# Kernel optimization log

Hardware: AMD Instinct MI355X
Metric: run time of the kernel (lower is better)

Reference implementation:

```python
import jax, jax.numpy as jnp
import numpy as np

EPS = 1e-5
SLOPE = 0.01  # LeakyReLU default negative_slope
D_STATE = 16


def leaky(x):
    return jnp.where(x >= 0, x, SLOPE * x)


def instance_norm(x):
    # InstanceNorm3d(affine=False): normalize per (n, c) over spatial dims
    m = x.mean(axis=(2, 3, 4), keepdims=True)
    v = x.var(axis=(2, 3, 4), keepdims=True)
    return (x - m) * jax.lax.rsqrt(v + EPS)


def conv3d(x, w, b, groups=1, pad=0):
    y = jax.lax.conv_general_dilated(
        x, w, (1, 1, 1), [(pad, pad)] * 3,
        dimension_numbers=('NCDHW', 'OIDHW', 'NCDHW'),
        feature_group_count=groups)
    return y + b[None, :, None, None, None]


def conv_transpose2(x, w, b):
    # ConvTranspose3d(k=2, s=2): non-overlapping, so it is a pure einsum+interleave
    # x: [n,c,d,h,w], w: [c,o,2,2,2] (torch layout)
    y = jnp.einsum('ncdhw,coijk->nodihjwk', x, w)
    n, o, d, _, h, _, ww, _ = y.shape
    return y.reshape(n, o, 2 * d, 2 * h, 2 * ww) + b[None, :, None, None, None]


def selective_scan(u, dt, A, B, C, D):
    # u, dt: [b,l,d]; A: [d,n]; B, C: [b,l,n]; D: [d]
    dA = jnp.exp(dt[..., None] * A)                              # [b,l,d,n]
    dBu = dt[..., None] * B[:, :, None, :] * u[..., None]        # [b,l,d,n]

    def step(h, inp):
        dA_t, dBu_t, C_t = inp
        h = dA_t * h + dBu_t                                     # [b,d,n]
        y = jnp.einsum('bdn,bn->bd', h, C_t)
        return h, y

    h0 = jnp.zeros((u.shape[0],) + A.shape, u.dtype)
    _, ys = jax.lax.scan(
        step, h0,
        (dA.transpose(1, 0, 2, 3), dBu.transpose(1, 0, 2, 3), C.transpose(1, 0, 2)))
    return ys.transpose(1, 0, 2) + u * D                         # [b,l,d]


def mamba_block(x, in_proj_w, conv1d_w, conv1d_b, x_proj_w,
                dt_proj_w, dt_proj_b, A_log, D_param, out_proj_w):
    # x: [b,l,c]
    dt_rank = dt_proj_w.shape[1]
    xz = x @ in_proj_w.T                                         # [b,l,2*d_inner]
    xi, z = jnp.split(xz, 2, axis=-1)
    # causal depthwise conv1d over sequence (torch pads d_conv-1 both sides, keeps [:L])
    xi_c = xi.transpose(0, 2, 1)                                 # [b,d_inner,l]
    xi_c = jax.lax.conv_general_dilated(
        xi_c, conv1d_w, (1,), [(conv1d_w.shape[-1] - 1, 0)],
        dimension_numbers=('NCH', 'OIH', 'NCH'),
        feature_group_count=xi_c.shape[1])
    xi = jax.nn.silu(xi_c + conv1d_b[None, :, None]).transpose(0, 2, 1)  # [b,l,d_inner]
    x_dbl = xi @ x_proj_w.T
    dt, B, C = jnp.split(x_dbl, [dt_rank, dt_rank + D_STATE], axis=-1)
    dt = jax.nn.softplus(dt @ dt_proj_w.T + dt_proj_b)
    A = -jnp.exp(A_log)
    y = selective_scan(xi, dt, A, B, C, D_param)
    y = y * jax.nn.silu(z)
    return y @ out_proj_w.T


def layer_norm(x, w, b):
    m = x.mean(-1, keepdims=True)
    v = x.var(-1, keepdims=True)
    return (x - m) * jax.lax.rsqrt(v + EPS) * w + b


def up_forward(x1, x2, up_w, up_b, dc1_w, dc1_b, dc2_w, dc2_b, dc3_w, dc3_b,
               ln_w, ln_b, in_proj_w, conv1d_w, conv1d_b, x_proj_w,
               dt_proj_w, dt_proj_b, A_log, D_param, out_proj_w):
    x1 = conv_transpose2(x1, up_w, up_b)
    dZ = x2.shape[2] - x1.shape[2]
    dY = x2.shape[3] - x1.shape[3]
    dX = x2.shape[4] - x1.shape[4]
    x1 = jnp.pad(x1, ((0, 0), (0, 0),
                      (dZ // 2, dZ - dZ // 2),
                      (dY // 2, dY - dY // 2),
                      (dX // 2, dX - dX // 2)))
    x = jnp.concatenate([x2, x1], axis=1)
    # DoubleConv (residual=False since in_channels != out_channels)
    x = leaky(instance_norm(conv3d(x, dc1_w, dc1_b)))
    x = leaky(instance_norm(conv3d(x, dc2_w, dc2_b, groups=8, pad=1)))
    x = leaky(instance_norm(conv3d(x, dc3_w, dc3_b)))
    # MambaLayer over flattened spatial tokens
    b, c, d, h, w = x.shape
    t = x.transpose(0, 2, 3, 4, 1).reshape(b, d * h * w, c)
    t = layer_norm(t, ln_w, ln_b)
    t = mamba_block(t, in_proj_w, conv1d_w, conv1d_b, x_proj_w,
                    dt_proj_w, dt_proj_b, A_log, D_param, out_proj_w)
    return t.reshape(b, d, h, w, c).transpose(0, 4, 1, 2, 3)


def setup_inputs() -> dict:
    key = jax.random.key(0)
    ks = jax.random.split(key, 20)
    c_out = 32      # out_channels / d_model
    d_inner = 64    # expand * d_model
    dt_rank = 2     # ceil(32/16)
    s = 0.02
    return {
        'x1': jax.random.normal(ks[0], (2, 32, 8, 16, 16), jnp.float32),
        'x2': jax.random.normal(ks[1], (2, 32, 16, 32, 32), jnp.float32),
        'up_w': jax.random.normal(ks[2], (32, 32, 2, 2, 2), jnp.float32) * s,
        'up_b': jnp.zeros((32,), jnp.float32),
        'dc1_w': jax.random.normal(ks[3], (32, 64, 1, 1, 1), jnp.float32) * s,
        'dc1_b': jnp.zeros((32,), jnp.float32),
        'dc2_w': jax.random.normal(ks[4], (32, 4, 3, 3, 3), jnp.float32) * s,
        'dc2_b': jnp.zeros((32,), jnp.float32),
        'dc3_w': jax.random.normal(ks[5], (32, 32, 1, 1, 1), jnp.float32) * s,
        'dc3_b': jnp.zeros((32,), jnp.float32),
        'ln_w': jnp.ones((c_out,), jnp.float32),
        'ln_b': jnp.zeros((c_out,), jnp.float32),
        'in_proj_w': jax.random.normal(ks[6], (2 * d_inner, c_out), jnp.float32) * s,
        'conv1d_w': jax.random.normal(ks[7], (d_inner, 1, 4), jnp.float32) * s,
        'conv1d_b': jnp.zeros((d_inner,), jnp.float32),
        'x_proj_w': jax.random.normal(ks[8], (dt_rank + 2 * D_STATE, d_inner), jnp.float32) * s,
        'dt_proj_w': jax.random.normal(ks[9], (d_inner, dt_rank), jnp.float32) * s,
        'dt_proj_b': jnp.full((d_inner,), -4.0, jnp.float32),
        'A_log': jnp.log(jnp.tile(jnp.arange(1.0, D_STATE + 1.0, dtype=jnp.float32), (d_inner, 1))),
        'D_param': jnp.ones((d_inner,), jnp.float32),
        'out_proj_w': jax.random.normal(ks[10], (c_out, d_inner), jnp.float32) * s,
    }


def reference(x1, x2, up_w, up_b, dc1_w, dc1_b, dc2_w, dc2_b, dc3_w, dc3_b,
              ln_w, ln_b, in_proj_w, conv1d_w, conv1d_b, x_proj_w,
              dt_proj_w, dt_proj_b, A_log, D_param, out_proj_w):
    return up_forward(x1, x2, up_w, up_b, dc1_w, dc1_b, dc2_w, dc2_b, dc3_w, dc3_b,
                      ln_w, ln_b, in_proj_w, conv1d_w, conv1d_b, x_proj_w,
                      dt_proj_w, dt_proj_b, A_log, D_param, out_proj_w)
```

## Files before the change

kernel.cpp:

```cpp
#include <hip/hip_runtime.h>

#define TPB 256
#define S_TOT 16384
#define NCHUNK 512
#define CLEN 32
#define EPS 1e-5f
#define SLOPE 0.01f

__device__ __forceinline__ float leakyf(float v){ return v > 0.f ? v : SLOPE * v; }
__device__ __forceinline__ float siluf(float v){ return v / (1.f + __expf(-v)); }

__global__ __launch_bounds__(TPB) void k_upc1(
    const float* __restrict__ x1, const float* __restrict__ x2,
    const float* __restrict__ upw, const float* __restrict__ upb,
    const float* __restrict__ w1, const float* __restrict__ b1,
    float* __restrict__ c1, float* st1p) {
  __shared__ float wq[8192];
  __shared__ float sup[64*33];
  __shared__ float red[4][8][2];
  int t = threadIdx.x, bid = blockIdx.x;
  int sb = bid & 255, n = bid >> 8;
  int p = t & 63, os = t >> 6;
  int s = sb*64 + p;
  for (int i = t; i < 8192; i += TPB) wq[i] = upw[i];
  __syncthreads();
  int z = s >> 10, y = (s >> 5) & 31, x = s & 31;
  int tap = ((z & 1)*2 + (y & 1))*2 + (x & 1);
  int xb = n*65536 + (z >> 1)*256 + (y >> 1)*16 + (x >> 1);
  float xv[32];
  #pragma unroll
  for (int c = 0; c < 32; c++) xv[c] = x1[xb + c*2048];
  float up[8];
  #pragma unroll
  for (int j = 0; j < 8; j++) up[j] = upb[os*8 + j];
  #pragma unroll
  for (int c = 0; c < 32; c++) {
    #pragma unroll
    for (int j = 0; j < 8; j++)
      up[j] += xv[c] * wq[c*256 + (os*8 + j)*8 + tap];
  }
  #pragma unroll
  for (int j = 0; j < 8; j++) sup[p*33 + os*8 + j] = up[j];
  __syncthreads();
  int c0 = os*8;
  float acc[8];
  #pragma unroll
  for (int j = 0; j < 8; j++) acc[j] = b1[c0 + j];
  const float* px2 = x2 + n*32*S_TOT + s;
  #pragma unroll
  for (int i = 0; i < 32; i++) {
    float v = px2[i*S_TOT];
    #pragma unroll
    for (int j = 0; j < 8; j++) acc[j] += v * w1[(c0 + j)*64 + i];
  }
  #pragma unroll
  for (int o = 0; o < 32; o++) {
    float v = sup[p*33 + o];
    #pragma unroll
    for (int j = 0; j < 8; j++) acc[j] += v * w1[(c0 + j)*64 + 32 + o];
  }
  #pragma unroll
  for (int j = 0; j < 8; j++)
    c1[(n*32 + c0 + j)*S_TOT + s] = acc[j];
  int wv = t >> 6;
  #pragma unroll
  for (int j = 0; j < 8; j++) {
    float sm = acc[j], sq = acc[j]*acc[j];
    #pragma unroll
    for (int o = 32; o > 0; o >>= 1) { sm += __shfl_down(sm, o); sq += __shfl_down(sq, o); }
    if ((t & 63) == 0) { red[wv][j][0] = sm; red[wv][j][1] = sq; }
  }
  __syncthreads();
  if (t < 64) {
    int w2 = t >> 4, j = (t >> 1) & 7, m = t & 1;
    st1p[((n*32 + w2*8 + j)*2 + m)*256 + sb] = red[w2][j][m];
  }
}

__global__ __launch_bounds__(TPB) void k_conv2(
    const float* __restrict__ c1, const float* __restrict__ w,
    const float* __restrict__ bias, const float* st1p,
    float* __restrict__ c2, float* st2p) {
  __shared__ float ws[432];
  __shared__ float tile[4080];
  __shared__ float smom[4][2];
  __shared__ float mrs[4][2];
  __shared__ float red[4][4][2];
  int bid = blockIdx.x, t = threadIdx.x;
  int sb = bid & 63, g = (bid >> 6) & 7, n = bid >> 9;
  int s0 = sb << 8;
  int z = s0 >> 10, y0 = (s0 >> 5) & 31;
  for (int i = t; i < 432; i += TPB) ws[i] = w[g*432 + i];
  {
    int pp = t >> 5, l = t & 31;
    if (pp < 8) {
      int j = pp & 3, m = pp >> 2;
      const float* sp = st1p + ((n*32 + g*4 + j)*2 + m)*256;
      float v = 0.f;
      #pragma unroll
      for (int k = 0; k < 8; k++) v += sp[l + 32*k];
      v += __shfl_down(v, 16); v += __shfl_down(v, 8); v += __shfl_down(v, 4);
      v += __shfl_down(v, 2);  v += __shfl_down(v, 1);
      if (l == 0) smom[j][m] = v;
    }
  }
  __syncthreads();
  if (t < 4) {
    float m = smom[t][0] * (1.f/S_TOT);
    mrs[t][0] = m; mrs[t][1] = rsqrtf(smom[t][1]*(1.f/S_TOT) - m*m + EPS);
  }
  __syncthreads();
  const float* cbase = c1 + (n*32 + g*4)*S_TOT;
  for (int i = t; i < 4080; i += TPB) {
    int ic = i / 1020, r = i - ic*1020;
    int zo = r / 340, r2 = r - zo*340;
    int yo = r2 / 34, xo = r2 - yo*34;
    int zz = z + zo - 1, yy = y0 + yo - 1, xx = xo - 1;
    float v = 0.f;
    if (zz >= 0 && zz < 16 && yy >= 0 && yy < 32 && xx >= 0 && xx < 32)
      v = leakyf((cbase[ic*S_TOT + zz*1024 + yy*32 + xx] - mrs[ic][0]) * mrs[ic][1]);
    tile[i] = v;
  }
  __syncthreads();
  int ty = t >> 5, x = t & 31;
  int s = s0 + t;
  float acc[4];
  #pragma unroll
  for (int oc = 0; oc < 4; oc++) acc[oc] = bias[g*4 + oc];
  #pragma unroll
  for (int ic = 0; ic < 4; ic++) {
    #pragma unroll
    for (int dz = 0; dz < 3; dz++) {
      #pragma unroll
      for (int dy = 0; dy < 3; dy++) {
        const float* tr = tile + ((ic*3 + dz)*10 + ty + dy)*34 + x;
        float p0 = tr[0], p1 = tr[1], p2 = tr[2];
        int wb = ic*27 + dz*9 + dy*3;
        #pragma unroll
        for (int oc = 0; oc < 4; oc++) {
          const float* wo = &ws[oc*108 + wb];
          acc[oc] += p0*wo[0] + p1*wo[1] + p2*wo[2];
        }
      }
    }
  }
  float sm[4], sq[4];
  #pragma unroll
  for (int oc = 0; oc < 4; oc++) {
    c2[(n*32 + g*4 + oc)*S_TOT + s] = acc[oc];
    sm[oc] = acc[oc]; sq[oc] = acc[oc]*acc[oc];
  }
  #pragma unroll
  for (int o = 32; o > 0; o >>= 1) {
    #pragma unroll
    for (int oc = 0; oc < 4; oc++) {
      sm[oc] += __shfl_down(sm[oc], o);
      sq[oc] += __shfl_down(sq[oc], o);
    }
  }
  int lane = t & 63, wv = t >> 6;
  if (lane == 0) {
    #pragma unroll
    for (int oc = 0; oc < 4; oc++) { red[wv][oc][0] = sm[oc]; red[wv][oc][1] = sq[oc]; }
  }
  __syncthreads();
  if (t < 8) {
    int oc = t & 3, m = t >> 2;
    float a = red[0][oc][m] + red[1][oc][m] + red[2][oc][m] + red[3][oc][m];
    st2p[((n*32 + g*4 + oc)*2 + m)*64 + sb] = a;
  }
}

__global__ __launch_bounds__(TPB) void k_conv3(
    const float* __restrict__ c2, const float* __restrict__ w,
    const float* __restrict__ bias, const float* st2p,
    float* __restrict__ c3, float* st3p) {
  __shared__ float ws[256];
  __shared__ float ssum[32][2];
  __shared__ float mrs[32][2];
  __shared__ float red[4][8][2];
  int t = threadIdx.x;
  int idx = blockIdx.x * TPB + t;
  int s = idx & 16383;
  int n = (idx >> 14) & 1;
  int q = idx >> 15;
  int sb = blockIdx.x & 63;
  int c0 = q*8;
  if (t < 256) ws[t] = w[c0*32 + t];
  if (t < 64) {
    int c = t >> 1, m = t & 1;
    const float* sp = st2p + ((n*32 + c)*2 + m)*64;
    float v = 0.f;
    #pragma unroll
    for (int k = 0; k < 64; k++) v += sp[k];
    ssum[c][m] = v;
  }
  __syncthreads();
  if (t < 32) {
    float m = ssum[t][0] * (1.f/S_TOT);
    mrs[t][0] = m; mrs[t][1] = rsqrtf(ssum[t][1]*(1.f/S_TOT) - m*m + EPS);
  }
  __syncthreads();
  const float* pin = c2 + n*32*S_TOT + s;
  float acc[8];
  #pragma unroll
  for (int j = 0; j < 8; j++) acc[j] = bias[c0 + j];
  #pragma unroll
  for (int i = 0; i < 32; i++) {
    float v = leakyf((pin[i*S_TOT] - mrs[i][0]) * mrs[i][1]);
    #pragma unroll
    for (int j = 0; j < 8; j++) acc[j] += v * ws[j*32 + i];
  }
  #pragma unroll
  for (int j = 0; j < 8; j++)
    c3[(n*32 + c0 + j)*S_TOT + s] = acc[j];
  int wv = t >> 6;
  #pragma unroll
  for (int j = 0; j < 8; j++) {
    float sm = acc[j], sq = acc[j]*acc[j];
    #pragma unroll
    for (int o = 32; o > 0; o >>= 1) { sm += __shfl_down(sm, o); sq += __shfl_down(sq, o); }
    if ((t & 63) == 0) { red[wv][j][0] = sm; red[wv][j][1] = sq; }
  }
  __syncthreads();
  if (t < 16) {
    int j = t >> 1, m = t & 1;
    float a = red[0][j][m] + red[1][j][m] + red[2][j][m] + red[3][j][m];
    st3p[((n*32 + c0 + j)*2 + m)*64 + sb] = a;
  }
}

__global__ __launch_bounds__(TPB) void k_token(
    const float* __restrict__ c3, const float* st3p,
    const float* __restrict__ lnw, const float* __restrict__ lnb,
    const float* __restrict__ ipw, const float* __restrict__ c1w,
    const float* __restrict__ c1b, const float* __restrict__ xpw,
    const float* __restrict__ dtw, const float* __restrict__ dtbi,
    const float* __restrict__ Alog,
    float* __restrict__ zb, float* __restrict__ u, float* __restrict__ dt,
    float* __restrict__ Bb, float* __restrict__ Cc,
    float* __restrict__ cA, float* __restrict__ cX) {
  __shared__ float un[4224];
  __shared__ float xpf[3264];
  __shared__ float sxi[2240];
  __shared__ float lnwb[64];
  __shared__ float mrs[64];
  __shared__ float ssum[64];
  float* Wraw = un;
  float* tk   = un;
  float* mv   = un + 1280;
  float* su2  = un;
  float* xd   = un + 2176;
  float* sdt2 = sxi;

  int t = threadIdx.x, bid = blockIdx.x;
  int tok0 = bid * 32;
  int n = tok0 >> 14, s0 = tok0 & 16383;
  int chunk = bid & (NCHUNK - 1);

  if (t < 64) {
    int c = t >> 1, m = t & 1;
    const float* sp = st3p + ((n*32 + c)*2 + m)*64;
    float v = 0.f;
    #pragma unroll
    for (int k = 0; k < 64; k++) v += sp[k];
    ssum[c*2 + m] = v;
  }
  for (int i = t; i < 4096; i += TPB) {
    int f = i >> 5, c = i & 31;
    Wraw[f*33 + c] = ipw[i];
  }
  for (int i = t; i < 3264; i += TPB) {
    int f = i / 68, dd = i - f*68;
    xpf[i] = (f < 34 && dd < 64) ? xpw[f*64 + dd] : 0.f;
  }
  if (t < 32) { lnwb[t] = lnw[t]; lnwb[32 + t] = lnb[t]; }
  __syncthreads();
  if (t < 32) {
    float m = ssum[t*2] * (1.f/S_TOT);
    mrs[t*2] = m; mrs[t*2 + 1] = rsqrtf(ssum[t*2 + 1]*(1.f/S_TOT) - m*m + EPS);
  }
  int fr = t & 127, half = t >> 7;
  float wreg[32];
  float S1 = 0.f, S2 = 0.f;
  #pragma unroll
  for (int c = 0; c < 32; c++) {
    float wa = Wraw[fr*33 + c];
    wreg[c] = wa * lnwb[c];
    S1 += wreg[c];
    S2 += wa * lnwb[32 + c];
  }
  __syncthreads();
  for (int i = t; i < 1120; i += TPB) {
    int c = i / 35, lt = i - c*35;
    int sg = s0 - 3 + lt;
    int sgc = sg < 0 ? 0 : sg;
    float raw = c3[(n*32 + c)*S_TOT + sgc];
    tk[lt*36 + c] = leakyf((raw - mrs[c*2]) * mrs[c*2 + 1]);
  }
  __syncthreads();
  if (t < 35) {
    float mean = 0.f;
    #pragma unroll
    for (int c = 0; c < 32; c++) mean += tk[t*36 + c];
    mean *= (1.f/32.f);
    float var = 0.f;
    #pragma unroll
    for (int c = 0; c < 32; c++) { float d2 = tk[t*36 + c] - mean; var += d2*d2; }
    mv[t*2] = mean; mv[t*2 + 1] = rsqrtf(var*(1.f/32.f) + EPS);
  }
  __syncthreads();
  for (int lt = half; lt < 35; lt += 2) {
    float acc = 0.f;
    #pragma unroll
    for (int c4 = 0; c4 < 8; c4++) {
      float4 tq = *(const float4*)(tk + lt*36 + 4*c4);
      acc += wreg[4*c4]*tq.x + wreg[4*c4+1]*tq.y + wreg[4*c4+2]*tq.z + wreg[4*c4+3]*tq.w;
    }
    float mean = mv[lt*2], rst = mv[lt*2 + 1];
    float r = rst*(acc - mean*S1) + S2;
    int sg = s0 - 3 + lt;
    if (fr < 64) {
      sxi[lt*64 + fr] = (sg < 0) ? 0.f : r;
    } else if (lt >= 3) {
      zb[(tok0 + lt - 3)*64 + (fr - 64)] = r;
    }
  }
  __syncthreads();
  int ch = t & 63;
  {
    float cw0 = c1w[ch*4], cw1 = c1w[ch*4+1], cw2 = c1w[ch*4+2], cw3 = c1w[ch*4+3];
    float cb = c1b[ch];
    #pragma unroll
    for (int r = 0; r < 8; r++) {
      int lt = (t >> 6) + 4*r;
      float acc = cb + sxi[lt*64 + ch]*cw0 + sxi[(lt+1)*64 + ch]*cw1
                     + sxi[(lt+2)*64 + ch]*cw2 + sxi[(lt+3)*64 + ch]*cw3;
      float uv = siluf(acc);
      u[(tok0 + lt)*64 + ch] = uv;
      su2[lt*68 + ch] = uv;
    }
  }
  __syncthreads();
  #pragma unroll
  for (int pass = 0; pass < 2; pass++) {
    int lt = (t >> 4) + pass*16;
    int f0 = (t & 15)*3;
    const float* sr = su2 + lt*68;
    const float* xr0 = xpf + f0*68;
    const float* xr1 = xpf + (f0+1)*68;
    const float* xr2 = xpf + (f0+2)*68;
    float a0 = 0.f, a1 = 0.f, a2 = 0.f;
    #pragma unroll
    for (int c4 = 0; c4 < 16; c4++) {
      float4 uq = *(const float4*)(sr + 4*c4);
      float4 q0 = *(const float4*)(xr0 + 4*c4);
      float4 q1 = *(const float4*)(xr1 + 4*c4);
      float4 q2 = *(const float4*)(xr2 + 4*c4);
      a0 += uq.x*q0.x + uq.y*q0.y + uq.z*q0.z + uq.w*q0.w;
      a1 += uq.x*q1.x + uq.y*q1.y + uq.z*q1.z + uq.w*q1.w;
      a2 += uq.x*q2.x + uq.y*q2.y + uq.z*q2.z + uq.w*q2.w;
    }
    if (f0     < 34) xd[lt*34 + f0]     = a0;
    if (f0 + 1 < 34) xd[lt*34 + f0 + 1] = a1;
    if (f0 + 2 < 34) xd[lt*34 + f0 + 2] = a2;
  }
  __syncthreads();
  {
    float dw0 = dtw[ch*2], dw1 = dtw[ch*2+1], db = dtbi[ch];
    #pragma unroll
    for (int r = 0; r < 8; r++) {
      int lt = (t >> 6) + 4*r;
      int token = tok0 + lt;
      float dv = xd[lt*34]*dw0 + xd[lt*34 + 1]*dw1 + db;
      float sp = fmaxf(dv, 0.f) + log1pf(__expf(-fabsf(dv)));
      dt[token*64 + ch] = sp;
      sdt2[lt*64 + ch] = sp;
      if (ch < 16)      Bb[token*16 + ch]      = xd[lt*34 + 2 + ch];
      else if (ch < 32) Cc[token*16 + ch - 16] = xd[lt*34 + 2 + ch];
    }
  }
  __syncthreads();
  {
    int q = t & 3, d = t >> 2;
    float Ar0 = -__expf(Alog[d*16 + 4*q]);
    float Ar1 = -__expf(Alog[d*16 + 4*q + 1]);
    float Ar2 = -__expf(Alog[d*16 + 4*q + 2]);
    float Ar3 = -__expf(Alog[d*16 + 4*q + 3]);
    float h0 = 0.f, h1 = 0.f, h2 = 0.f, h3 = 0.f, sdts = 0.f;
    #pragma unroll 4
    for (int tt = 0; tt < CLEN; tt++) {
      float dtv = sdt2[tt*64 + d], uv = su2[tt*68 + d];
      sdts += dtv;
      float du = dtv * uv;
      const float* bp = xd + tt*34 + 2 + 4*q;
      float B0 = bp[0], B1 = bp[1], B2 = bp[2], B3 = bp[3];
      h0 = __expf(Ar0*dtv)*h0 + B0*du;
      h1 = __expf(Ar1*dtv)*h1 + B1*du;
      h2 = __expf(Ar2*dtv)*h2 + B2*du;
      h3 = __expf(Ar3*dtv)*h3 + B3*du;
    }
    int base = (n*NCHUNK + chunk)*1024 + 4*t;
    float4 av; av.x = __expf(Ar0*sdts); av.y = __expf(Ar1*sdts);
    av.z = __expf(Ar2*sdts); av.w = __expf(Ar3*sdts);
    float4 xv4; xv4.x = h0; xv4.y = h1; xv4.z = h2; xv4.w = h3;
    *(float4*)(cA + base) = av;
    *(float4*)(cX + base) = xv4;
  }
}


__global__ __launch_bounds__(TPB) void k_scan2(
    const float* __restrict__ cA, float* __restrict__ cX) {
  int t = threadIdx.x;
  int w = blockIdx.x*4 + (t >> 6);
  int lane = t & 63;
  int b = w >> 10, e = w & 1023;
  size_t base = (size_t)b*NCHUNK*1024 + e;
  float a[8], x[8];
  #pragma unroll
  for (int k = 0; k < 8; k++) {
    size_t idx = base + (size_t)(lane*8 + k)*1024;
    a[k] = cA[idx];
    x[k] = cX[idx];
  }
  float A = 1.f, X = 0.f;
  #pragma unroll
  for (int k = 0; k < 8; k++) { X = X*a[k] + x[k]; A *= a[k]; }
  #pragma unroll
  for (int off = 1; off < 64; off <<= 1) {
    float Ap = __shfl_up(A, off);
    float Xp = __shfl_up(X, off);
    if (lane >= off) { X = A*Xp + X; A = A*Ap; }
  }
  float Xe = __shfl_up(X, 1);
  if (lane == 0) Xe = 0.f;
  float r = Xe;
  #pragma unroll
  for (int k = 0; k < 8; k++) {
    size_t idx = base + (size_t)(lane*8 + k)*1024;
    cX[idx] = r;
    r = a[k]*r + x[k];
  }
}

__global__ __launch_bounds__(TPB) void k_scan3(
    const float* __restrict__ dt, const float* __restrict__ u,
    const float* __restrict__ Bb, const float* __restrict__ Cc,
    const float* __restrict__ Alog, const float* __restrict__ Dp,
    const float* __restrict__ zb, const float* __restrict__ cX,
    const float* __restrict__ opw, float* __restrict__ out) {
  __shared__ __align__(16) float sdt[1024], su[1024], sB[256], sC[256];
  __shared__ float gt[32*65];
  int bid = blockIdx.x, t = threadIdx.x;
  int chunk = bid & (NCHUNK-1), b = bid >> 9;
  int q = t & 3, d = t >> 2;
  float Ar[4];
  #pragma unroll
  for (int j = 0; j < 4; j++) Ar[j] = -__expf(Alog[d*16 + 4*q + j]);
  float h[4];
  {
    float4 hs = *(const float4*)(cX + (size_t)(b*NCHUNK + chunk)*1024 + 4*t);
    h[0] = hs.x; h[1] = hs.y; h[2] = hs.z; h[3] = hs.w;
  }
  float Dv = Dp[d];
  int tg0 = b*S_TOT + chunk*CLEN;
  for (int tile = 0; tile < 2; tile++) {
    int base = tg0 + tile*16;
    {
      int i = t*4;
      *(float4*)(sdt + i) = *(const float4*)(dt + base*64 + i);
      *(float4*)(su  + i) = *(const float4*)(u  + base*64 + i);
    }
    for (int i = t; i < 1024; i += TPB)
      gt[(tile*16 + (i >> 6))*65 + (i & 63)] = zb[base*64 + i];
    sB[t] = Bb[base*16 + t];
    sC[t] = Cc[base*16 + t];
    __syncthreads();
    #pragma unroll
    for (int tt = 0; tt < 16; tt++) {
      float dtv = sdt[tt*64 + d], uv = su[tt*64 + d];
      float du = dtv * uv;
      float4 Bq = *(const float4*)(sB + tt*16 + q*4);
      float4 Cq = *(const float4*)(sC + tt*16 + q*4);
      h[0] = __expf(Ar[0]*dtv)*h[0] + Bq.x*du;
      h[1] = __expf(Ar[1]*dtv)*h[1] + Bq.y*du;
      h[2] = __expf(Ar[2]*dtv)*h[2] + Bq.z*du;
      h[3] = __expf(Ar[3]*dtv)*h[3] + Bq.w*du;
      float yp = h[0]*Cq.x + h[1]*Cq.y + h[2]*Cq.z + h[3]*Cq.w;
      yp += __shfl_xor(yp, 1);
      yp += __shfl_xor(yp, 2);
      if (q == 0) {
        float zv = gt[(tile*16 + tt)*65 + d];
        gt[(tile*16 + tt)*65 + d] = (yp + uv*Dv) * siluf(zv);
      }
    }
    __syncthreads();
  }
  {
    int sl = t & 31, cb = t >> 5;
    float acc[4] = {0.f,0.f,0.f,0.f};
    const float* wp = opw + cb*4*64;
    #pragma unroll
    for (int dd = 0; dd < 64; dd++) {
      float v = gt[sl*65 + dd];
      #pragma unroll
      for (int j = 0; j < 4; j++) acc[j] += v * wp[j*64 + dd];
    }
    #pragma unroll
    for (int j = 0; j < 4; j++)
      out[(b*32 + cb*4 + j)*S_TOT + chunk*CLEN + sl] = acc[j];
  }
}

extern "C" void kernel_launch(void* const* d_in, const int* in_sizes, int n_in,
                              void* d_out, int out_size, void* d_ws, size_t ws_size,
                              hipStream_t stream) {
  const float* x1    = (const float*)d_in[0];
  const float* x2    = (const float*)d_in[1];
  const float* upw   = (const float*)d_in[2];
  const float* upb   = (const float*)d_in[3];
  const float* dc1w  = (const float*)d_in[4];
  const float* dc1b  = (const float*)d_in[5];
  const float* dc2w  = (const float*)d_in[6];
  const float* dc2b  = (const float*)d_in[7];
  const float* dc3w  = (const float*)d_in[8];
  const float* dc3b  = (const float*)d_in[9];
  const float* lnw   = (const float*)d_in[10];
  const float* lnb   = (const float*)d_in[11];
  const float* ipw   = (const float*)d_in[12];
  const float* c1w   = (const float*)d_in[13];
  const float* c1b   = (const float*)d_in[14];
  const float* xpw   = (const float*)d_in[15];
  const float* dtw   = (const float*)d_in[16];
  const float* dtbi  = (const float*)d_in[17];
  const float* Alog  = (const float*)d_in[18];
  const float* Dp    = (const float*)d_in[19];
  const float* opw   = (const float*)d_in[20];
  float* out = (float*)d_out;

  float* ws = (float*)d_ws;
  float* st1p  = ws + 0;
  float* st2p  = ws + 32768;
  float* st3p  = ws + 40960;
  float* c1    = ws + 49152;
  float* c2    = ws + 1097728;
  float* c3    = ws + 2146304;
  float* zb    = ws + 3194880;
  float* ub    = ws + 5292032;
  float* dtb   = ws + 7389184;
  float* Bb    = ws + 9486336;
  float* Cc    = ws + 10010624;
  float* cA    = ws + 10534912;
  float* cX    = ws + 11583488;

  k_upc1 <<<512,  TPB, 0, stream>>>(x1, x2, upw, upb, dc1w, dc1b, c1, st1p);
  k_conv2<<<1024, TPB, 0, stream>>>(c1, dc2w, dc2b, st1p, c2, st2p);
  k_conv3<<<512,  TPB, 0, stream>>>(c2, dc3w, dc3b, st2p, c3, st3p);
  k_token<<<1024, TPB, 0, stream>>>(c3, st3p, lnw, lnb, ipw, c1w, c1b, xpw,
                                    dtw, dtbi, Alog, zb, ub, dtb, Bb, Cc, cA, cX);
  k_scan2<<<512,  TPB, 0, stream>>>(cA, cX);
  k_scan3<<<1024, TPB, 0, stream>>>(dtb, ub, Bb, Cc, Alog, Dp, zb, cX, opw, out);
}
```

Measured before the change: 234.2 us.

## Replace wave-parallel chunk scan with per-thread sequential scan over chunks

Result: slower. 246.7 us (+5.3%).

```diff
diff --git a/kernel.cpp b/kernel.cpp
--- a/kernel.cpp
+++ b/kernel.cpp
@@ -412,35 +412,16 @@
 
 __global__ __launch_bounds__(TPB) void k_scan2(
     const float* __restrict__ cA, float* __restrict__ cX) {
-  int t = threadIdx.x;
-  int w = blockIdx.x*4 + (t >> 6);
-  int lane = t & 63;
-  int b = w >> 10, e = w & 1023;
+  int tid = blockIdx.x*TPB + threadIdx.x;
+  int b = tid >> 10, e = tid & 1023;
   size_t base = (size_t)b*NCHUNK*1024 + e;
-  float a[8], x[8];
-  #pragma unroll
-  for (int k = 0; k < 8; k++) {
-    size_t idx = base + (size_t)(lane*8 + k)*1024;
-    a[k] = cA[idx];
-    x[k] = cX[idx];
-  }
-  float A = 1.f, X = 0.f;
-  #pragma unroll
-  for (int k = 0; k < 8; k++) { X = X*a[k] + x[k]; A *= a[k]; }
-  #pragma unroll
-  for (int off = 1; off < 64; off <<= 1) {
-    float Ap = __shfl_up(A, off);
-    float Xp = __shfl_up(X, off);
-    if (lane >= off) { X = A*Xp + X; A = A*Ap; }
-  }
-  float Xe = __shfl_up(X, 1);
-  if (lane == 0) Xe = 0.f;
-  float r = Xe;
-  #pragma unroll
-  for (int k = 0; k < 8; k++) {
-    size_t idx = base + (size_t)(lane*8 + k)*1024;
-    cX[idx] = r;
-    r = a[k]*r + x[k];
+  float h = 0.f;
+  #pragma unroll 8
+  for (int c = 0; c < NCHUNK; c++) {
+    size_t idx = base + (size_t)c*1024;
+    float a = cA[idx], x = cX[idx];
+    cX[idx] = h;
+    h = a*h + x;
   }
 }
 
@@ -559,6 +540,6 @@
   k_conv3<<<512,  TPB, 0, stream>>>(c2, dc3w, dc3b, st2p, c3, st3p);
   k_token<<<1024, TPB, 0, stream>>>(c3, st3p, lnw, lnb, ipw, c1w, c1b, xpw,
                                     dtw, dtbi, Alog, zb, ub, dtb, Bb, Cc, cA, cX);
-  k_scan2<<<512,  TPB, 0, stream>>>(cA, cX);
+  k_scan2<<<8,    TPB, 0, stream>>>(cA, cX);
   k_scan3<<<1024, TPB, 0, stream>>>(dtb, ub, Bb, Cc, Alog, Dp, zb, cX, opw, out);
 }
```
